# Optimization experiments

Measured on AMD Instinct MI355X. Metric: run time of the kernel, lower is better.

The kernel has to match this reference:

```python
import jax, jax.numpy as jnp
import numpy as np

WS = 16          # window_size
HS = 8           # halo_size
NH = 4           # num_heads
DIM = 128
WSH = WS + 2 * HS  # 32, window with halo
B, H, W = 2, 128, 128


def _rel_pos_index():
    # static relative-position index table, (WSH^2, WSH^2), int
    r = np.arange(-HS, WS + HS)
    coords = np.stack(np.meshgrid(r, r, indexing='ij'))        # (2, WSH, WSH)
    cf = coords.reshape(2, -1)                                  # (2, WSH^2)
    rel = (cf[:, :, None] - cf[:, None, :]).transpose(1, 2, 0)  # (L, L, 2)
    rel = rel.copy()
    rel[..., 0] += WS + HS - 1
    rel[..., 1] += WS + HS - 1
    rel[..., 0] *= 2 * WS + 2 * HS - 1
    return rel.sum(-1)  # (1024, 1024)

_RPI = _rel_pos_index()


def setup_inputs() -> dict:
    key = jax.random.key(0)
    ks = jax.random.split(key, 10)
    p = lambda k, shp: (jax.random.normal(k, shp, dtype=jnp.float32) * 0.02)
    return {
        'x': jax.random.normal(ks[0], (B, H, W, DIM), dtype=jnp.float32),
        'Wq': p(ks[1], (DIM, DIM)), 'bq': jnp.zeros((DIM,), jnp.float32),
        'Wk': p(ks[2], (DIM, DIM)), 'bk': jnp.zeros((DIM,), jnp.float32),
        'Wv': p(ks[3], (DIM, DIM)), 'bv': jnp.zeros((DIM,), jnp.float32),
        'Wp': p(ks[4], (DIM, DIM)), 'bp': jnp.zeros((DIM,), jnp.float32),
        'bias_table': p(ks[5], ((2 * WS + 2 * HS - 1) ** 2, NH)),
        'shift_size': 0,
    }


def reference(x, Wq, bq, Wk, bk, Wv, bv, Wp, bp, bias_table, shift_size):
    Bx, Hx, Wx, C = x.shape
    hd = C // NH
    scale = hd ** -0.5
    if shift_size > 0:
        x = jnp.roll(x, (-shift_size, -shift_size), axis=(1, 2))
    # reflect-pad by halo and gather overlapping 32x32 windows (stride 16)
    xp = jnp.pad(x, ((0, 0), (HS, HS), (HS, HS), (0, 0)), mode='reflect')
    nWh, nWw = Hx // WS, Wx // WS
    rows = (jnp.arange(nWh) * WS)[:, None] + jnp.arange(WSH)   # (nWh, 32)
    cols = (jnp.arange(nWw) * WS)[:, None] + jnp.arange(WSH)   # (nWw, 32)
    w = xp[:, rows]                 # (B, nWh, 32, Wp, C)
    w = w[:, :, :, cols]            # (B, nWh, 32, nWw, 32, C)
    w = w.transpose(0, 1, 3, 2, 4, 5).reshape(-1, WSH, WSH, C)  # (B*nW, 32, 32, C)
    center = w[:, HS:HS + WS, HS:HS + WS].reshape(-1, WS * WS, C)   # (nWb, 256, C)
    kv = w.reshape(-1, WSH * WSH, C)                                # (nWb, 1024, C)
    q = (center @ Wq.T + bq).reshape(-1, WS * WS, NH, hd).transpose(0, 2, 1, 3)
    k = (kv @ Wk.T + bk).reshape(-1, WSH * WSH, NH, hd).transpose(0, 2, 1, 3)
    v = (kv @ Wv.T + bv).reshape(-1, WSH * WSH, NH, hd).transpose(0, 2, 1, 3)
    attn = jnp.einsum('bhqd,bhkd->bhqk', q, k) * scale   # (nWb, H, 256, 1024)
    bias = bias_table[_RPI.reshape(-1)].reshape(WSH * WSH, WSH * WSH, NH)
    bias = bias.transpose(2, 0, 1)                        # (H, 1024, 1024)
    start = HS * 2 * WS                                   # 256, as in source
    attn = attn + bias[:, start:start + WS * WS, :][None]
    attn = jax.nn.softmax(attn, axis=-1)
    out = jnp.einsum('bhqk,bhkd->bhqd', attn, v)
    out = out.transpose(0, 2, 1, 3).reshape(-1, WS * WS, C)
    out = out @ Wp.T + bp
    out = out.reshape(Bx, nWh, nWw, WS, WS, C).transpose(0, 1, 3, 2, 4, 5)
    out = out.reshape(Bx, Hx, Wx, C)
    if shift_size > 0:
        out = jnp.roll(out, (shift_size, shift_size), axis=(1, 2))
    return out
```

## Files before the change

kernel.cpp:

```cpp
#include <hip/hip_runtime.h>


typedef unsigned short ushort_t;
typedef __attribute__((ext_vector_type(8))) short bf16x8;
typedef __attribute__((ext_vector_type(4))) float floatx4;

#define NHEADS 4
#define BTBL 2209
#define PK 64
#define LOG2E 1.4426950408889634f
#define QSCALE (0.17677669529663687f * LOG2E)

__device__ __forceinline__ int reflect_idx(int p) {
    p = (p < 0) ? -p : p;
    p = (p > 127) ? 254 - p : p;
    return p;
}

__device__ __forceinline__ ushort_t f2b(float x) {
    unsigned u = __float_as_uint(x);
    return (ushort_t)((u + 0x7fffu + ((u >> 16) & 1u)) >> 16);
}

__global__ __launch_bounds__(256) void prep(
    const float* __restrict__ Wq, const float* __restrict__ Wk,
    const float* __restrict__ Wv, const float* __restrict__ Wp,
    const float* __restrict__ bq, const float* __restrict__ bk,
    const float* __restrict__ bv, const float* __restrict__ bp,
    const float* __restrict__ bt,
    ushort_t* __restrict__ Wqkv, ushort_t* __restrict__ Wpb,
    float* __restrict__ bqkv, float* __restrict__ bpb,
    ushort_t* __restrict__ bf)
{
    if (blockIdx.x < 257) {
        int idx = blockIdx.x * 256 + threadIdx.x;
        if (idx < 16384)       Wqkv[idx] = f2b(Wq[idx]);
        else if (idx < 32768)  Wqkv[idx] = f2b(Wk[idx - 16384]);
        else if (idx < 49152)  Wqkv[idx] = f2b(Wv[idx - 32768]);
        else if (idx < 65536)  Wpb[idx - 49152] = f2b(Wp[idx - 49152]);
        else {
            int e = idx - 65536;
            for (int k = e; k < 512; k += 256) {
                if (k < 128)      bqkv[k] = bq[k];
                else if (k < 256) bqkv[k] = bk[k - 128];
                else if (k < 384) bqkv[k] = bv[k - 256];
                else              bpb[k - 384] = bp[k - 384];
            }
        }
    } else {
        int idx  = (blockIdx.x - 257) * 256 + threadIdx.x;
        int lane = idx & 63;
        int qtw  = (idx >> 6) & 15;
        int kt   = (idx >> 10) & 63;
        int h    = (idx >> 16) & 3;
        int q     = qtw * 16 + (lane & 15);
        int kbase = kt * 16 + ((lane >> 4) << 2);
        unsigned v[4];
        #pragma unroll
        for (int r = 0; r < 4; ++r) {
            int key = kbase + r;
            int kr = key >> 5, kc = key & 31;
            int bidx = ((q >> 5) + 31 - kr) * 47 + (q & 31) - kc + 23;
            if (bidx < 0) bidx += BTBL;
            v[r] = f2b(bt[bidx * NHEADS + h] * LOG2E);
        }
        uint2 out;
        out.x = v[0] | (v[1] << 16);
        out.y = v[2] | (v[3] << 16);
        *(uint2*)&bf[(size_t)idx * 4] = out;
    }
}

template <bool IN_BF16, bool OUT_BF16, int NB>
__global__ __launch_bounds__(256) void gemm_mfma(
    const void* __restrict__ Xv, const ushort_t* __restrict__ W,
    const float* __restrict__ bias, void* __restrict__ Yv,
    const int ldy, const float scale0)
{
    __shared__ ushort_t Xs[128 * 136];

    const int t    = threadIdx.x;
    const int w    = t >> 6;
    const int lane = t & 63;
    const int quad = lane >> 4;
    const int l15  = lane & 15;
    const int m0   = blockIdx.x * 128;

    if (IN_BF16) {
        const ushort_t* X = (const ushort_t*)Xv;
        #pragma unroll
        for (int i = 0; i < 8; ++i) {
            int s = t + i * 256;
            int row = s >> 4, c8 = s & 15;
            *(int4*)&Xs[row * 136 + c8 * 8] =
                *(const int4*)&X[(size_t)(m0 + row) * 128 + c8 * 8];
        }
    } else {
        const float* X = (const float*)Xv;
        #pragma unroll
        for (int i = 0; i < 16; ++i) {
            int s = t + i * 256;
            int row = s >> 5, c4 = s & 31;
            float4 v = *(const float4*)&X[(size_t)(m0 + row) * 128 + c4 * 4];
            uint2 pk;
            pk.x = (unsigned)f2b(v.x) | ((unsigned)f2b(v.y) << 16);
            pk.y = (unsigned)f2b(v.z) | ((unsigned)f2b(v.w) << 16);
            *(uint2*)&Xs[row * 136 + c4 * 4] = pk;
        }
    }
    __syncthreads();

    #pragma unroll 1
    for (int nb = 0; nb < NB; ++nb) {
        const float sc = (nb == 0) ? scale0 : 1.0f;

        floatx4 acc[2][8];
        #pragma unroll
        for (int nt = 0; nt < 8; ++nt) {
            floatx4 bv = *(const floatx4*)&bias[nb * 128 + nt * 16 + quad * 4];
            acc[0][nt] = bv;
            acc[1][nt] = bv;
        }

        #pragma unroll
        for (int kc = 0; kc < 4; ++kc) {
            bf16x8 af[2], bfr[8];
            #pragma unroll
            for (int mt = 0; mt < 2; ++mt)
                af[mt] = *(const bf16x8*)&Xs[(w * 32 + mt * 16 + l15) * 136 + kc * 32 + quad * 8];
            #pragma unroll
            for (int nt = 0; nt < 8; ++nt)
                bfr[nt] = *(const bf16x8*)&W[(size_t)(nb * 128 + nt * 16 + l15) * 128 + kc * 32 + quad * 8];
            #pragma unroll
            for (int mt = 0; mt < 2; ++mt)
                #pragma unroll
                for (int nt = 0; nt < 8; ++nt)
                    acc[mt][nt] = __builtin_amdgcn_mfma_f32_16x16x32_bf16(bfr[nt], af[mt], acc[mt][nt], 0, 0, 0);
        }

        #pragma unroll
        for (int mt = 0; mt < 2; ++mt) {
            int m = m0 + w * 32 + mt * 16 + l15;
            #pragma unroll
            for (int nt = 0; nt < 8; ++nt) {
                int n = nb * 128 + nt * 16 + quad * 4;
                if (OUT_BF16) {
                    uint2 pk;
                    pk.x = (unsigned)f2b(acc[mt][nt][0] * sc) |
                           ((unsigned)f2b(acc[mt][nt][1] * sc) << 16);
                    pk.y = (unsigned)f2b(acc[mt][nt][2] * sc) |
                           ((unsigned)f2b(acc[mt][nt][3] * sc) << 16);
                    *(uint2*)&((ushort_t*)Yv)[(size_t)m * ldy + n] = pk;
                } else {
                    float4 v;
                    v.x = acc[mt][nt][0] * sc; v.y = acc[mt][nt][1] * sc;
                    v.z = acc[mt][nt][2] * sc; v.w = acc[mt][nt][3] * sc;
                    *(float4*)&((float*)Yv)[(size_t)m * ldy + n] = v;
                }
            }
        }
    }
}

__global__ __launch_bounds__(256, 2) void halo_attn(
    const ushort_t* __restrict__ QKV,
    const ushort_t* __restrict__ biasf,
    ushort_t* __restrict__ O)
{
    __shared__ ushort_t P_lds[4 * 64 * PK];
    __shared__ ushort_t Vt_lds[4 * 32 * PK];

    const int t    = threadIdx.x;
    const int wave = t >> 6;
    const int lane = t & 63;
    const int quad = lane >> 4;
    const int l15  = lane & 15;
    const int swz  = (l15 & 7) << 3;

    const int win  = blockIdx.x;
    const int head = blockIdx.y;
    const int b    = win >> 6;
    const int wh   = (win >> 3) & 7;
    const int ww   = win & 7;

    bf16x8 qf[4];
    int qpix[4];
    #pragma unroll
    for (int qt = 0; qt < 4; ++qt) {
        int q_abs = wave * 64 + qt * 16 + l15;
        int gy = wh * 16 + (q_abs >> 4), gx = ww * 16 + (q_abs & 15);
        int pix = (b * 128 + gy) * 128 + gx;
        qpix[qt] = pix;
        qf[qt] = *(const bf16x8*)(QKV + (size_t)pix * 384 + head * 32 + quad * 8);
    }

    floatx4 Oa[2][4];
    #pragma unroll
    for (int dt = 0; dt < 2; ++dt)
        #pragma unroll
        for (int qt = 0; qt < 4; ++qt)
            Oa[dt][qt] = (floatx4)0.f;
    float l[4] = {0.f, 0.f, 0.f, 0.f};

    ushort_t* Pw  = P_lds  + wave * 64 * PK;
    ushort_t* Vtw = Vt_lds + wave * 32 * PK;

    for (int c = 0; c < 16; ++c) {
        {
            int keyv = c * 64 + lane;
            int ky = reflect_idx(wh * 16 + (keyv >> 5) - 8);
            int kx = reflect_idx(ww * 16 + (keyv & 31) - 8);
            int pixv = (b * 128 + ky) * 128 + kx;
            const int4* vp4 = (const int4*)(QKV + (size_t)pixv * 384 + 256 + head * 32);
            int4 vw0 = vp4[0], vw1 = vp4[1], vw2 = vp4[2], vw3 = vp4[3];
            const ushort_t* vs0 = (const ushort_t*)&vw0;
            const ushort_t* vs1 = (const ushort_t*)&vw1;
            const ushort_t* vs2 = (const ushort_t*)&vw2;
            const ushort_t* vs3 = (const ushort_t*)&vw3;
            #pragma unroll
            for (int d = 0; d < 8; ++d) {
                int cs = lane ^ (d << 3);
                Vtw[(d +  0) * PK + cs] = vs0[d];
                Vtw[(d +  8) * PK + cs] = vs1[d];
                Vtw[(d + 16) * PK + cs] = vs2[d];
                Vtw[(d + 24) * PK + cs] = vs3[d];
            }
        }

        bf16x8 kf[4];
        #pragma unroll
        for (int kt = 0; kt < 4; ++kt) {
            int key = c * 64 + kt * 16 + l15;
            int ky = reflect_idx(wh * 16 + (key >> 5) - 8);
            int kx = reflect_idx(ww * 16 + (key & 31) - 8);
            int pixk = (b * 128 + ky) * 128 + kx;
            kf[kt] = *(const bf16x8*)(QKV + (size_t)pixk * 384 + 128 + head * 32 + quad * 8);
        }

        floatx4 S[4][4];
        #pragma unroll
        for (int kt = 0; kt < 4; ++kt) {
            int kt_abs = c * 4 + kt;
            #pragma unroll
            for (int qt = 0; qt < 4; ++qt) {
                size_t off = ((((size_t)head * 64 + kt_abs) * 16 + (wave * 4 + qt)) * 64 + lane) * 4;
                uint2 bb = *(const uint2*)(biasf + off);
                floatx4 s;
                s[0] = __uint_as_float(bb.x << 16);
                s[1] = __uint_as_float(bb.x & 0xffff0000u);
                s[2] = __uint_as_float(bb.y << 16);
                s[3] = __uint_as_float(bb.y & 0xffff0000u);
                S[kt][qt] = s;
            }
        }
        #pragma unroll
        for (int kt = 0; kt < 4; ++kt)
            #pragma unroll
            for (int qt = 0; qt < 4; ++qt)
                S[kt][qt] = __builtin_amdgcn_mfma_f32_16x16x32_bf16(kf[kt], qf[qt], S[kt][qt], 0, 0, 0);

        #pragma unroll
        for (int qt = 0; qt < 4; ++qt) {
            float ls = 0.f;
            #pragma unroll
            for (int kt = 0; kt < 4; ++kt) {
                #pragma unroll
                for (int r = 0; r < 4; ++r) {
                    float p = __builtin_amdgcn_exp2f(S[kt][qt][r]);
                    S[kt][qt][r] = p;
                    ls += p;
                }
            }
            l[qt] += ls;
            #pragma unroll
            for (int kt = 0; kt < 4; ++kt) {
                uint2 pk;
                pk.x = __builtin_amdgcn_perm(__float_as_uint(S[kt][qt][1]),
                                             __float_as_uint(S[kt][qt][0]), 0x07060302u);
                pk.y = __builtin_amdgcn_perm(__float_as_uint(S[kt][qt][3]),
                                             __float_as_uint(S[kt][qt][2]), 0x07060302u);
                *(uint2*)&Pw[(qt * 16 + l15) * PK + ((kt * 16 + quad * 4) ^ swz)] = pk;
            }
        }

        #pragma unroll
        for (int ks = 0; ks < 2; ++ks) {
            bf16x8 vf[2];
            #pragma unroll
            for (int dt = 0; dt < 2; ++dt)
                vf[dt] = *(const bf16x8*)&Vtw[(dt * 16 + l15) * PK + ((ks * 32 + quad * 8) ^ swz)];
            #pragma unroll
            for (int qt = 0; qt < 4; ++qt) {
                bf16x8 pf = *(const bf16x8*)&Pw[(qt * 16 + l15) * PK + ((ks * 32 + quad * 8) ^ swz)];
                #pragma unroll
                for (int dt = 0; dt < 2; ++dt)
                    Oa[dt][qt] = __builtin_amdgcn_mfma_f32_16x16x32_bf16(vf[dt], pf, Oa[dt][qt], 0, 0, 0);
            }
        }
    }

    #pragma unroll
    for (int qt = 0; qt < 4; ++qt) {
        float lq = l[qt];
        lq += __shfl_xor(lq, 16);
        lq += __shfl_xor(lq, 32);
        float inv = 1.0f / lq;
        #pragma unroll
        for (int dt = 0; dt < 2; ++dt) {
            uint2 pk;
            pk.x = (unsigned)f2b(Oa[dt][qt][0] * inv) | ((unsigned)f2b(Oa[dt][qt][1] * inv) << 16);
            pk.y = (unsigned)f2b(Oa[dt][qt][2] * inv) | ((unsigned)f2b(Oa[dt][qt][3] * inv) << 16);
            *(uint2*)(O + (size_t)qpix[qt] * 128 + head * 32 + dt * 16 + quad * 4) = pk;
        }
    }
}

extern "C" void kernel_launch(void* const* d_in, const int* in_sizes, int n_in,
                              void* d_out, int out_size, void* d_ws, size_t ws_size,
                              hipStream_t stream)
{
    const float* x          = (const float*)d_in[0];
    const float* Wq         = (const float*)d_in[1];
    const float* bq         = (const float*)d_in[2];
    const float* Wk         = (const float*)d_in[3];
    const float* bk         = (const float*)d_in[4];
    const float* Wv         = (const float*)d_in[5];
    const float* bv         = (const float*)d_in[6];
    const float* Wp         = (const float*)d_in[7];
    const float* bp         = (const float*)d_in[8];
    const float* bias_table = (const float*)d_in[9];
    float* out = (float*)d_out;

    char* ws = (char*)d_ws;
    ushort_t* Wqkv = (ushort_t*)(ws);
    ushort_t* Wpb  = (ushort_t*)(ws + 98304);
    float*    bqkv = (float*)   (ws + 131072);
    float*    bpb  = (float*)   (ws + 132608);
    ushort_t* QKV  = (ushort_t*)(ws + 133120);
    ushort_t* Ob   = (ushort_t*)(ws + 25298944);
    ushort_t* bf   = (ushort_t*)(ws + 33687552);

    prep<<<dim3(1281), dim3(256), 0, stream>>>(Wq, Wk, Wv, Wp, bq, bk, bv, bp,
                                               bias_table, Wqkv, Wpb, bqkv, bpb, bf);
    gemm_mfma<false, true, 3><<<dim3(256), dim3(256), 0, stream>>>(
        x, Wqkv, bqkv, QKV, 384, QSCALE);
    halo_attn<<<dim3(128, NHEADS), dim3(256), 0, stream>>>(QKV, bf, Ob);
    gemm_mfma<true, false, 1><<<dim3(256), dim3(256), 0, stream>>>(
        Ob, Wpb, bpb, out, 128, 1.0f);
}
```

Baseline: 167.5 us.

## Share V tile across waves and software-pipeline PV with next chunk's QK/exp

Previously each wave loaded and transposed its own full copy of the V chunk into LDS. Now the four waves split the V load (each handles an 8-dim slice) into one shared, double-buffered V tile, and P is double-buffered per wave. The loop is restructured so the PV MFMAs of chunk c-1 run alongside V staging and the QK/exp of chunk c, with one block barrier per iteration. s_setprio hints are added around the MFMA sections. This cuts redundant global V traffic by four and overlaps memory latency with compute, at the cost of a block-wide barrier per chunk and more LDS use.

```diff
diff --git a/kernel.cpp b/kernel.cpp
--- a/kernel.cpp
+++ b/kernel.cpp
@@ -167,8 +167,8 @@
     const ushort_t* __restrict__ biasf,
     ushort_t* __restrict__ O)
 {
-    __shared__ ushort_t P_lds[4 * 64 * PK];
-    __shared__ ushort_t Vt_lds[4 * 32 * PK];
+    __shared__ ushort_t P_lds[4][2][64 * PK];
+    __shared__ ushort_t Vt_lds[2][32 * PK];
 
     const int t    = threadIdx.x;
     const int wave = t >> 6;
@@ -182,6 +182,11 @@
     const int b    = win >> 6;
     const int wh   = (win >> 3) & 7;
     const int ww   = win & 7;
+
+    const int vkey = t & 63;
+    const int vchk = t >> 6;
+    const int vrow = vkey >> 5;
+    const int vkx  = reflect_idx(ww * 16 + (vkey & 31) - 8);
 
     bf16x8 qf[4];
     int qpix[4];
@@ -202,31 +207,20 @@
             Oa[dt][qt] = (floatx4)0.f;
     float l[4] = {0.f, 0.f, 0.f, 0.f};
 
-    ushort_t* Pw  = P_lds  + wave * 64 * PK;
-    ushort_t* Vtw = Vt_lds + wave * 32 * PK;
-
-    for (int c = 0; c < 16; ++c) {
-        {
-            int keyv = c * 64 + lane;
-            int ky = reflect_idx(wh * 16 + (keyv >> 5) - 8);
-            int kx = reflect_idx(ww * 16 + (keyv & 31) - 8);
-            int pixv = (b * 128 + ky) * 128 + kx;
-            const int4* vp4 = (const int4*)(QKV + (size_t)pixv * 384 + 256 + head * 32);
-            int4 vw0 = vp4[0], vw1 = vp4[1], vw2 = vp4[2], vw3 = vp4[3];
-            const ushort_t* vs0 = (const ushort_t*)&vw0;
-            const ushort_t* vs1 = (const ushort_t*)&vw1;
-            const ushort_t* vs2 = (const ushort_t*)&vw2;
-            const ushort_t* vs3 = (const ushort_t*)&vw3;
-            #pragma unroll
-            for (int d = 0; d < 8; ++d) {
-                int cs = lane ^ (d << 3);
-                Vtw[(d +  0) * PK + cs] = vs0[d];
-                Vtw[(d +  8) * PK + cs] = vs1[d];
-                Vtw[(d + 16) * PK + cs] = vs2[d];
-                Vtw[(d + 24) * PK + cs] = vs3[d];
-            }
-        }
-
+    auto stageV = [&](int c, int par) {
+        int ky = reflect_idx(wh * 16 + 2 * c + vrow - 8);
+        int pixv = (b * 128 + ky) * 128 + vkx;
+        int4 vw = *(const int4*)(QKV + (size_t)pixv * 384 + 256 + head * 32 + vchk * 8);
+        const ushort_t* vs = (const ushort_t*)&vw;
+        ushort_t* Vp = &Vt_lds[par][0];
+        #pragma unroll
+        for (int j = 0; j < 8; ++j) {
+            int d = vchk * 8 + j;
+            Vp[d * PK + (vkey ^ (j << 3))] = vs[j];
+        }
+    };
+
+    auto sExp = [&](int c, int par) {
         bf16x8 kf[4];
         #pragma unroll
         for (int kt = 0; kt < 4; ++kt) {
@@ -236,7 +230,6 @@
             int pixk = (b * 128 + ky) * 128 + kx;
             kf[kt] = *(const bf16x8*)(QKV + (size_t)pixk * 384 + 128 + head * 32 + quad * 8);
         }
-
         floatx4 S[4][4];
         #pragma unroll
         for (int kt = 0; kt < 4; ++kt) {
@@ -253,12 +246,15 @@
                 S[kt][qt] = s;
             }
         }
+        __builtin_amdgcn_s_setprio(1);
         #pragma unroll
         for (int kt = 0; kt < 4; ++kt)
             #pragma unroll
             for (int qt = 0; qt < 4; ++qt)
                 S[kt][qt] = __builtin_amdgcn_mfma_f32_16x16x32_bf16(kf[kt], qf[qt], S[kt][qt], 0, 0, 0);
-
+        __builtin_amdgcn_s_setprio(0);
+
+        ushort_t* Pw = &P_lds[wave][par][0];
         #pragma unroll
         for (int qt = 0; qt < 4; ++qt) {
             float ls = 0.f;
@@ -282,13 +278,18 @@
                 *(uint2*)&Pw[(qt * 16 + l15) * PK + ((kt * 16 + quad * 4) ^ swz)] = pk;
             }
         }
-
+    };
+
+    auto pv = [&](int par) {
+        const ushort_t* Vp = &Vt_lds[par][0];
+        const ushort_t* Pw = &P_lds[wave][par][0];
+        __builtin_amdgcn_s_setprio(1);
         #pragma unroll
         for (int ks = 0; ks < 2; ++ks) {
             bf16x8 vf[2];
             #pragma unroll
             for (int dt = 0; dt < 2; ++dt)
-                vf[dt] = *(const bf16x8*)&Vtw[(dt * 16 + l15) * PK + ((ks * 32 + quad * 8) ^ swz)];
+                vf[dt] = *(const bf16x8*)&Vp[(dt * 16 + l15) * PK + ((ks * 32 + quad * 8) ^ swz)];
             #pragma unroll
             for (int qt = 0; qt < 4; ++qt) {
                 bf16x8 pf = *(const bf16x8*)&Pw[(qt * 16 + l15) * PK + ((ks * 32 + quad * 8) ^ swz)];
@@ -297,7 +298,23 @@
                     Oa[dt][qt] = __builtin_amdgcn_mfma_f32_16x16x32_bf16(vf[dt], pf, Oa[dt][qt], 0, 0, 0);
             }
         }
-    }
+        __builtin_amdgcn_s_setprio(0);
+    };
+
+    stageV(0, 0);
+    sExp(0, 0);
+    asm volatile("s_waitcnt lgkmcnt(0)" ::: "memory");
+    __builtin_amdgcn_s_barrier();
+
+    for (int c = 1; c < 16; ++c) {
+        int par = c & 1;
+        stageV(c, par);
+        pv(par ^ 1);
+        sExp(c, par);
+        asm volatile("s_waitcnt lgkmcnt(0)" ::: "memory");
+        __builtin_amdgcn_s_barrier();
+    }
+    pv(1);
 
     #pragma unroll
     for (int qt = 0; qt < 4; ++qt) {
```

Result: no change. 168.5 us (+0.6%).

## Fuse prep, QKV GEMM, attention and projection into one cooperative kernel

Applied to the files above, without the earlier changes.

Replaces the four separate launches (weight/bias prep, QKV projection, halo attention, output projection) with a single cooperative kernel of 512 blocks that separates stages with grid-wide syncs. It aims to remove per-launch overhead and inter-kernel gaps. The GEMM stages now use 64-row tiles across 512 blocks, and attention maps one window-head per block. In exchange it adds three grid barriers and requires every block to be co-resident, with a fallback to the old multi-kernel path if the cooperative launch fails.

```diff
diff --git a/kernel.cpp b/kernel.cpp
--- a/kernel.cpp
+++ b/kernel.cpp
@@ -1,5 +1,8 @@
 #include <hip/hip_runtime.h>
-
+#include <hip/hip_cooperative_groups.h>
+
+
+namespace cg = cooperative_groups;
 
 typedef unsigned short ushort_t;
 typedef __attribute__((ext_vector_type(8))) short bf16x8;
@@ -20,6 +23,303 @@
 __device__ __forceinline__ ushort_t f2b(float x) {
     unsigned u = __float_as_uint(x);
     return (ushort_t)((u + 0x7fffu + ((u >> 16) & 1u)) >> 16);
+}
+
+__global__ __launch_bounds__(256, 2) void halo_fused(
+    const float* __restrict__ x,
+    const float* __restrict__ Wq, const float* __restrict__ Wk,
+    const float* __restrict__ Wv, const float* __restrict__ Wp,
+    const float* __restrict__ bq, const float* __restrict__ bk,
+    const float* __restrict__ bv, const float* __restrict__ bp,
+    const float* __restrict__ bt,
+    ushort_t* __restrict__ Wqkv, ushort_t* __restrict__ Wpb,
+    float* __restrict__ bqkv, float* __restrict__ bpb,
+    ushort_t* __restrict__ QKV, ushort_t* __restrict__ Ob,
+    ushort_t* __restrict__ biasf, float* __restrict__ out)
+{
+    __shared__ ushort_t smem[24576];
+
+    const int bid  = blockIdx.x;
+    const int t    = threadIdx.x;
+    const int wave = t >> 6;
+    const int lane = t & 63;
+    const int quad = lane >> 4;
+    const int l15  = lane & 15;
+
+    cg::grid_group grid = cg::this_grid();
+
+    if (bid < 257) {
+        int idx = bid * 256 + t;
+        if (idx < 16384)       Wqkv[idx] = f2b(Wq[idx]);
+        else if (idx < 32768)  Wqkv[idx] = f2b(Wk[idx - 16384]);
+        else if (idx < 49152)  Wqkv[idx] = f2b(Wv[idx - 32768]);
+        else if (idx < 65536)  Wpb[idx - 49152] = f2b(Wp[idx - 49152]);
+        else {
+            int e = idx - 65536;
+            for (int k = e; k < 512; k += 256) {
+                if (k < 128)      bqkv[k] = bq[k];
+                else if (k < 256) bqkv[k] = bk[k - 128];
+                else if (k < 384) bqkv[k] = bv[k - 256];
+                else              bpb[k - 384] = bp[k - 384];
+            }
+        }
+    }
+    #pragma unroll
+    for (int j = 0; j < 2; ++j) {
+        int idx = bid * 512 + j * 256 + t;
+        int ln  = idx & 63;
+        int qtw = (idx >> 6) & 15;
+        int kt  = (idx >> 10) & 63;
+        int h   = (idx >> 16) & 3;
+        int q     = qtw * 16 + (ln & 15);
+        int kbase = kt * 16 + ((ln >> 4) << 2);
+        unsigned v[4];
+        #pragma unroll
+        for (int r = 0; r < 4; ++r) {
+            int key = kbase + r;
+            int kr = key >> 5, kc = key & 31;
+            int bidx = ((q >> 5) + 31 - kr) * 47 + (q & 31) - kc + 23;
+            if (bidx < 0) bidx += BTBL;
+            v[r] = f2b(bt[bidx * NHEADS + h] * LOG2E);
+        }
+        uint2 o;
+        o.x = v[0] | (v[1] << 16);
+        o.y = v[2] | (v[3] << 16);
+        *(uint2*)&biasf[(size_t)idx * 4] = o;
+    }
+    __threadfence();
+    grid.sync();
+
+    {
+        const int m0 = bid * 64;
+        #pragma unroll
+        for (int i = 0; i < 8; ++i) {
+            int s = t + i * 256;
+            int row = s >> 5, c4 = s & 31;
+            float4 v = *(const float4*)&x[(size_t)(m0 + row) * 128 + c4 * 4];
+            uint2 pk;
+            pk.x = (unsigned)f2b(v.x) | ((unsigned)f2b(v.y) << 16);
+            pk.y = (unsigned)f2b(v.z) | ((unsigned)f2b(v.w) << 16);
+            *(uint2*)&smem[row * 136 + c4 * 4] = pk;
+        }
+        __syncthreads();
+
+        #pragma unroll 1
+        for (int nb = 0; nb < 3; ++nb) {
+            const float sc = (nb == 0) ? QSCALE : 1.0f;
+            floatx4 acc[8];
+            #pragma unroll
+            for (int nt = 0; nt < 8; ++nt)
+                acc[nt] = *(const floatx4*)&bqkv[nb * 128 + nt * 16 + quad * 4];
+
+            #pragma unroll
+            for (int kc = 0; kc < 4; ++kc) {
+                bf16x8 af = *(const bf16x8*)&smem[(wave * 16 + l15) * 136 + kc * 32 + quad * 8];
+                bf16x8 bfr[8];
+                #pragma unroll
+                for (int nt = 0; nt < 8; ++nt)
+                    bfr[nt] = *(const bf16x8*)&Wqkv[(size_t)(nb * 128 + nt * 16 + l15) * 128 + kc * 32 + quad * 8];
+                #pragma unroll
+                for (int nt = 0; nt < 8; ++nt)
+                    acc[nt] = __builtin_amdgcn_mfma_f32_16x16x32_bf16(bfr[nt], af, acc[nt], 0, 0, 0);
+            }
+
+            int m = m0 + wave * 16 + l15;
+            #pragma unroll
+            for (int nt = 0; nt < 8; ++nt) {
+                int n = nb * 128 + nt * 16 + quad * 4;
+                uint2 pk;
+                pk.x = (unsigned)f2b(acc[nt][0] * sc) | ((unsigned)f2b(acc[nt][1] * sc) << 16);
+                pk.y = (unsigned)f2b(acc[nt][2] * sc) | ((unsigned)f2b(acc[nt][3] * sc) << 16);
+                *(uint2*)&QKV[(size_t)m * 384 + n] = pk;
+            }
+        }
+    }
+    __threadfence();
+    grid.sync();
+
+    {
+        ushort_t* P_lds  = smem;
+        ushort_t* Vt_lds = smem + 16384;
+        const int swz  = (l15 & 7) << 3;
+
+        const int win  = bid & 127;
+        const int head = bid >> 7;
+        const int b    = win >> 6;
+        const int wh   = (win >> 3) & 7;
+        const int ww   = win & 7;
+
+        bf16x8 qf[4];
+        int qpix[4];
+        #pragma unroll
+        for (int qt = 0; qt < 4; ++qt) {
+            int q_abs = wave * 64 + qt * 16 + l15;
+            int gy = wh * 16 + (q_abs >> 4), gx = ww * 16 + (q_abs & 15);
+            int pix = (b * 128 + gy) * 128 + gx;
+            qpix[qt] = pix;
+            qf[qt] = *(const bf16x8*)(QKV + (size_t)pix * 384 + head * 32 + quad * 8);
+        }
+
+        floatx4 Oa[2][4];
+        #pragma unroll
+        for (int dt = 0; dt < 2; ++dt)
+            #pragma unroll
+            for (int qt = 0; qt < 4; ++qt)
+                Oa[dt][qt] = (floatx4)0.f;
+        float l[4] = {0.f, 0.f, 0.f, 0.f};
+
+        ushort_t* Pw  = P_lds  + wave * 64 * PK;
+        ushort_t* Vtw = Vt_lds + wave * 32 * PK;
+
+        for (int c = 0; c < 16; ++c) {
+            {
+                int keyv = c * 64 + lane;
+                int ky = reflect_idx(wh * 16 + (keyv >> 5) - 8);
+                int kx = reflect_idx(ww * 16 + (keyv & 31) - 8);
+                int pixv = (b * 128 + ky) * 128 + kx;
+                const int4* vp4 = (const int4*)(QKV + (size_t)pixv * 384 + 256 + head * 32);
+                int4 vw0 = vp4[0], vw1 = vp4[1], vw2 = vp4[2], vw3 = vp4[3];
+                const ushort_t* vs0 = (const ushort_t*)&vw0;
+                const ushort_t* vs1 = (const ushort_t*)&vw1;
+                const ushort_t* vs2 = (const ushort_t*)&vw2;
+                const ushort_t* vs3 = (const ushort_t*)&vw3;
+                #pragma unroll
+                for (int d = 0; d < 8; ++d) {
+                    int cs = lane ^ (d << 3);
+                    Vtw[(d +  0) * PK + cs] = vs0[d];
+                    Vtw[(d +  8) * PK + cs] = vs1[d];
+                    Vtw[(d + 16) * PK + cs] = vs2[d];
+                    Vtw[(d + 24) * PK + cs] = vs3[d];
+                }
+            }
+
+            bf16x8 kf[4];
+            #pragma unroll
+            for (int kt = 0; kt < 4; ++kt) {
+                int key = c * 64 + kt * 16 + l15;
+                int ky = reflect_idx(wh * 16 + (key >> 5) - 8);
+                int kx = reflect_idx(ww * 16 + (key & 31) - 8);
+                int pixk = (b * 128 + ky) * 128 + kx;
+                kf[kt] = *(const bf16x8*)(QKV + (size_t)pixk * 384 + 128 + head * 32 + quad * 8);
+            }
+
+            floatx4 S[4][4];
+            #pragma unroll
+            for (int kt = 0; kt < 4; ++kt) {
+                int kt_abs = c * 4 + kt;
+                #pragma unroll
+                for (int qt = 0; qt < 4; ++qt) {
+                    size_t off = ((((size_t)head * 64 + kt_abs) * 16 + (wave * 4 + qt)) * 64 + lane) * 4;
+                    uint2 bb = *(const uint2*)(biasf + off);
+                    floatx4 s;
+                    s[0] = __uint_as_float(bb.x << 16);
+                    s[1] = __uint_as_float(bb.x & 0xffff0000u);
+                    s[2] = __uint_as_float(bb.y << 16);
+                    s[3] = __uint_as_float(bb.y & 0xffff0000u);
+                    S[kt][qt] = s;
+                }
+            }
+            #pragma unroll
+            for (int kt = 0; kt < 4; ++kt)
+                #pragma unroll
+                for (int qt = 0; qt < 4; ++qt)
+                    S[kt][qt] = __builtin_amdgcn_mfma_f32_16x16x32_bf16(kf[kt], qf[qt], S[kt][qt], 0, 0, 0);
+
+            #pragma unroll
+            for (int qt = 0; qt < 4; ++qt) {
+                float ls = 0.f;
+                #pragma unroll
+                for (int kt = 0; kt < 4; ++kt) {
+                    #pragma unroll
+                    for (int r = 0; r < 4; ++r) {
+                        float p = __builtin_amdgcn_exp2f(S[kt][qt][r]);
+                        S[kt][qt][r] = p;
+                        ls += p;
+                    }
+                }
+                l[qt] += ls;
+                #pragma unroll
+                for (int kt = 0; kt < 4; ++kt) {
+                    uint2 pk;
+                    pk.x = __builtin_amdgcn_perm(__float_as_uint(S[kt][qt][1]),
+                                                 __float_as_uint(S[kt][qt][0]), 0x07060302u);
+                    pk.y = __builtin_amdgcn_perm(__float_as_uint(S[kt][qt][3]),
+                                                 __float_as_uint(S[kt][qt][2]), 0x07060302u);
+                    *(uint2*)&Pw[(qt * 16 + l15) * PK + ((kt * 16 + quad * 4) ^ swz)] = pk;
+                }
+            }
+
+            #pragma unroll
+            for (int ks = 0; ks < 2; ++ks) {
+                bf16x8 vf[2];
+                #pragma unroll
+                for (int dt = 0; dt < 2; ++dt)
+                    vf[dt] = *(const bf16x8*)&Vtw[(dt * 16 + l15) * PK + ((ks * 32 + quad * 8) ^ swz)];
+                #pragma unroll
+                for (int qt = 0; qt < 4; ++qt) {
+                    bf16x8 pf = *(const bf16x8*)&Pw[(qt * 16 + l15) * PK + ((ks * 32 + quad * 8) ^ swz)];
+                    #pragma unroll
+                    for (int dt = 0; dt < 2; ++dt)
+                        Oa[dt][qt] = __builtin_amdgcn_mfma_f32_16x16x32_bf16(vf[dt], pf, Oa[dt][qt], 0, 0, 0);
+                }
+            }
+        }
+
+        #pragma unroll
+        for (int qt = 0; qt < 4; ++qt) {
+            float lq = l[qt];
+            lq += __shfl_xor(lq, 16);
+            lq += __shfl_xor(lq, 32);
+            float inv = 1.0f / lq;
+            #pragma unroll
+            for (int dt = 0; dt < 2; ++dt) {
+                uint2 pk;
+                pk.x = (unsigned)f2b(Oa[dt][qt][0] * inv) | ((unsigned)f2b(Oa[dt][qt][1] * inv) << 16);
+                pk.y = (unsigned)f2b(Oa[dt][qt][2] * inv) | ((unsigned)f2b(Oa[dt][qt][3] * inv) << 16);
+                *(uint2*)(Ob + (size_t)qpix[qt] * 128 + head * 32 + dt * 16 + quad * 4) = pk;
+            }
+        }
+    }
+    __threadfence();
+    grid.sync();
+
+    {
+        const int m0 = bid * 64;
+        #pragma unroll
+        for (int i = 0; i < 4; ++i) {
+            int s = t + i * 256;
+            int row = s >> 4, c8 = s & 15;
+            *(int4*)&smem[row * 136 + c8 * 8] =
+                *(const int4*)&Ob[(size_t)(m0 + row) * 128 + c8 * 8];
+        }
+        __syncthreads();
+
+        floatx4 acc[8];
+        #pragma unroll
+        for (int nt = 0; nt < 8; ++nt)
+            acc[nt] = *(const floatx4*)&bpb[nt * 16 + quad * 4];
+
+        #pragma unroll
+        for (int kc = 0; kc < 4; ++kc) {
+            bf16x8 af = *(const bf16x8*)&smem[(wave * 16 + l15) * 136 + kc * 32 + quad * 8];
+            bf16x8 bfr[8];
+            #pragma unroll
+            for (int nt = 0; nt < 8; ++nt)
+                bfr[nt] = *(const bf16x8*)&Wpb[(size_t)(nt * 16 + l15) * 128 + kc * 32 + quad * 8];
+            #pragma unroll
+            for (int nt = 0; nt < 8; ++nt)
+                acc[nt] = __builtin_amdgcn_mfma_f32_16x16x32_bf16(bfr[nt], af, acc[nt], 0, 0, 0);
+        }
+
+        int m = m0 + wave * 16 + l15;
+        #pragma unroll
+        for (int nt = 0; nt < 8; ++nt) {
+            int n = nt * 16 + quad * 4;
+            float4 v;
+            v.x = acc[nt][0]; v.y = acc[nt][1]; v.z = acc[nt][2]; v.w = acc[nt][3];
+            *(float4*)&out[(size_t)m * 128 + n] = v;
+        }
+    }
 }
 
 __global__ __launch_bounds__(256) void prep(
@@ -64,10 +364,10 @@
             if (bidx < 0) bidx += BTBL;
             v[r] = f2b(bt[bidx * NHEADS + h] * LOG2E);
         }
-        uint2 out;
-        out.x = v[0] | (v[1] << 16);
-        out.y = v[2] | (v[3] << 16);
-        *(uint2*)&bf[(size_t)idx * 4] = out;
+        uint2 o;
+        o.x = v[0] | (v[1] << 16);
+        o.y = v[2] | (v[3] << 16);
+        *(uint2*)&bf[(size_t)idx * 4] = o;
     }
 }
 
@@ -340,11 +640,27 @@
     ushort_t* Ob   = (ushort_t*)(ws + 25298944);
     ushort_t* bf   = (ushort_t*)(ws + 33687552);
 
-    prep<<<dim3(1281), dim3(256), 0, stream>>>(Wq, Wk, Wv, Wp, bq, bk, bv, bp,
-                                               bias_table, Wqkv, Wpb, bqkv, bpb, bf);
-    gemm_mfma<false, true, 3><<<dim3(256), dim3(256), 0, stream>>>(
-        x, Wqkv, bqkv, QKV, 384, QSCALE);
-    halo_attn<<<dim3(128, NHEADS), dim3(256), 0, stream>>>(QKV, bf, Ob);
-    gemm_mfma<true, false, 1><<<dim3(256), dim3(256), 0, stream>>>(
-        Ob, Wpb, bpb, out, 128, 1.0f);
+    const float *x_ = x, *Wq_ = Wq, *Wk_ = Wk, *Wv_ = Wv, *Wp_ = Wp;
+    const float *bq_ = bq, *bk_ = bk, *bv_ = bv, *bp_ = bp, *bt_ = bias_table;
+    ushort_t *Wqkv_ = Wqkv, *Wpb_ = Wpb, *QKV_ = QKV, *Ob_ = Ob, *bf_ = bf;
+    float *bqkv_ = bqkv, *bpb_ = bpb, *out_ = out;
+    void* kargs[] = {
+        (void*)&x_, (void*)&Wq_, (void*)&Wk_, (void*)&Wv_, (void*)&Wp_,
+        (void*)&bq_, (void*)&bk_, (void*)&bv_, (void*)&bp_, (void*)&bt_,
+        (void*)&Wqkv_, (void*)&Wpb_, (void*)&bqkv_, (void*)&bpb_,
+        (void*)&QKV_, (void*)&Ob_, (void*)&bf_, (void*)&out_ };
+
+    hipError_t err = hipLaunchCooperativeKernel(
+        (const void*)halo_fused, dim3(512), dim3(256), kargs, 0u, stream);
+
+    if (err != hipSuccess) {
+        (void)hipGetLastError();
+        prep<<<dim3(1281), dim3(256), 0, stream>>>(Wq, Wk, Wv, Wp, bq, bk, bv, bp,
+                                                   bias_table, Wqkv, Wpb, bqkv, bpb, bf);
+        gemm_mfma<false, true, 3><<<dim3(256), dim3(256), 0, stream>>>(
+            x, Wqkv, bqkv, QKV, 384, QSCALE);
+        halo_attn<<<dim3(128, NHEADS), dim3(256), 0, stream>>>(QKV, bf, Ob);
+        gemm_mfma<true, false, 1><<<dim3(256), dim3(256), 0, stream>>>(
+            Ob, Wpb, bpb, out, 128, 1.0f);
+    }
 }
```

After: 512.4 us. 206% more time.
